# Kernel optimization log

Measured on AMD Instinct MI355X. Metric: run time of the kernel, lower is better.

The kernel has to match this reference:

```python
import jax, jax.numpy as jnp
import numpy as np

V = 100000   # vocab size
H = 1280     # GRU hidden / pic_emb_size
E = 300      # word_emb_size
L = 32       # max_length


def setup_inputs() -> dict:
    key = jax.random.key(0)
    ks = jax.random.split(key, 7)
    s = 0.02  # weight init scale
    return {
        "hidden0": jax.random.normal(ks[0], (H,), jnp.float32),
        "start_emb": jax.random.normal(ks[1], (E,), jnp.float32),
        "W_ih": jax.random.normal(ks[2], (3 * H, E), jnp.float32) * s,
        "W_hh": jax.random.normal(ks[3], (3 * H, H), jnp.float32) * s,
        "b_ih": jnp.zeros((3 * H,), jnp.float32),
        "b_hh": jnp.zeros((3 * H,), jnp.float32),
        "W_cls": jax.random.normal(ks[4], (V, H), jnp.float32) * s,
        "b_cls": jnp.zeros((V,), jnp.float32),
        "vocab_vectors": jax.random.normal(ks[5], (V, E), jnp.float32),
        "max_length": L,
    }


def reference(hidden0, start_emb, W_ih, W_hh, b_ih, b_hh, W_cls, b_cls,
              vocab_vectors, max_length):
    """Autoregressive GRU decode: GRU step -> 1280x100k classifier GEMV ->
    argmax -> embedding gather, for max_length steps (batch=1).
    EOS (token 0) emulated with a `done` mask instead of a Python break.
    Returns (tokens [L] int32, hiddens [L, H] float32)."""

    def step(carry, _):
        h, emb, done = carry
        # PyTorch GRU gate layout: [reset | update | new]
        gi = W_ih @ emb + b_ih               # [3H]
        gh = W_hh @ h + b_hh                 # [3H]
        r = jax.nn.sigmoid(gi[:H] + gh[:H])
        z = jax.nn.sigmoid(gi[H:2 * H] + gh[H:2 * H])
        n = jnp.tanh(gi[2 * H:] + r * gh[2 * H:])
        h_new = jnp.where(done, h, (1.0 - z) * n + z * h)
        logits = W_cls @ h_new + b_cls       # [V] classifier GEMV
        pred = jnp.argmax(logits).astype(jnp.int32)
        token = jnp.where(done, 0, pred)
        done_new = done | (pred == 0)
        emb_new = jnp.where(done_new, emb, vocab_vectors[pred])  # gather next word emb
        return (h_new, emb_new, done_new), (token, h_new)

    init = (hidden0, start_emb, jnp.array(False))
    _, (tokens, hiddens) = jax.lax.scan(step, init, None, length=max_length)
    return tokens, hiddens
```

## Files before the change

### kernel.cpp

```cpp
#include <hip/hip_runtime.h>
#include <math.h>
#include <limits.h>

#define V 100000
#define H 1280
#define E 300
#define L 32
#define NBLK 1563

#define WS_H0     0
#define WS_H1     1280
#define WS_EMB    2560
#define WS_SUM8   2880
#define WS_DONE   3008
#define WS_LOGITS 3012
#define WS_SROW   (WS_LOGITS + V)
#define WS_PLO    (WS_SROW + V)
#define WS_PHI    (WS_PLO + NBLK)
#define WS_Q_BYTEOFF 824576
#define WS_BYTES_NEEDED (WS_Q_BYTEOFF + (size_t)V * H)
#define CAND_CAP  256
#define PBLK_CAP  128

#define FB_GI     4000
#define FB_GH     (FB_GI + 3840)
#define FB_NPART  6250
#define FB_PVAL   12000
#define FB_PIDX   (FB_PVAL + FB_NPART)

__global__ __launch_bounds__(256)
void init_state(const float* __restrict__ hidden0, const float* __restrict__ start_emb,
                float* __restrict__ ws) {
    int i = blockIdx.x * blockDim.x + threadIdx.x;
    if (i < H) ws[WS_H0 + i] = hidden0[i];
    if (i < E) ws[WS_EMB + i] = start_emb[i];
    if (i < 8) ws[WS_SUM8 + i * 16] = 0.f;
    if (i == 0) ((int*)ws)[WS_DONE] = 0;
}

__global__ __launch_bounds__(256)
void convert_int8(const float* __restrict__ W, uint* __restrict__ q_out,
                  float* __restrict__ ws) {
    const int wave = threadIdx.x >> 6;
    const int lane = threadIdx.x & 63;
    const int row = blockIdx.x * 4 + wave;
    const float4* __restrict__ wr = (const float4*)(W + (size_t)row * H);

    float4 v[5];
    float mx = 0.f;
    #pragma unroll
    for (int k = 0; k < 5; ++k) {
        v[k] = wr[lane + 64*k];
        mx = fmaxf(mx, fmaxf(fmaxf(fabsf(v[k].x), fabsf(v[k].y)),
                             fmaxf(fabsf(v[k].z), fabsf(v[k].w))));
    }
    #pragma unroll
    for (int off = 32; off; off >>= 1) mx = fmaxf(mx, __shfl_xor(mx, off));

    float inv = (mx > 0.f) ? 127.0f / mx : 0.f;
    float s   = (mx > 0.f) ? mx / 127.0f : 0.f;

    uint* __restrict__ qrow = q_out + (size_t)row * (H/4);
    #pragma unroll
    for (int k = 0; k < 5; ++k) {
        int q0 = max(-127, min(127, __float2int_rn(v[k].x * inv)));
        int q1 = max(-127, min(127, __float2int_rn(v[k].y * inv)));
        int q2 = max(-127, min(127, __float2int_rn(v[k].z * inv)));
        int q3 = max(-127, min(127, __float2int_rn(v[k].w * inv)));
        qrow[lane + 64*k] = (uint)(q0 & 0xff) | ((uint)(q1 & 0xff) << 8) |
                            ((uint)(q2 & 0xff) << 16) | ((uint)(q3 & 0xff) << 24);
    }
    if (lane == 0) ws[WS_SROW + row] = s;
}

__global__ __launch_bounds__(192)
void gru_fused(const float* __restrict__ W_ih, const float* __restrict__ W_hh,
               const float* __restrict__ b_ih, const float* __restrict__ b_hh,
               float* __restrict__ ws, const float* __restrict__ hin,
               float* __restrict__ hout, float* __restrict__ hid_out) {
    const int g = threadIdx.x >> 6;
    const int lane = threadIdx.x & 63;
    const int j = blockIdx.x;
    const int row = g * H + j;

    const float4* __restrict__ emb4 = (const float4*)(ws + WS_EMB);
    const float4* __restrict__ h4   = (const float4*)hin;

    const float4* __restrict__ wi = (const float4*)(W_ih + (size_t)row * E);
    float si = 0.f;
    for (int i = lane; i < 75; i += 64) {
        float4 w = wi[i], e = emb4[i];
        si += w.x*e.x + w.y*e.y + w.z*e.z + w.w*e.w;
    }
    const float4* __restrict__ wh = (const float4*)(W_hh + (size_t)row * H);
    float sh = 0.f;
    #pragma unroll
    for (int k = 0; k < 5; ++k) {
        float4 w = wh[lane + 64*k], hv = h4[lane + 64*k];
        sh += w.x*hv.x + w.y*hv.y + w.z*hv.z + w.w*hv.w;
    }
    #pragma unroll
    for (int off = 32; off; off >>= 1) {
        si += __shfl_down(si, off);
        sh += __shfl_down(sh, off);
    }
    __shared__ float gi_s[3], gh_s[3];
    if (lane == 0) {
        gi_s[g] = si + b_ih[row];
        gh_s[g] = sh + b_hh[row];
    }
    __syncthreads();
    if (threadIdx.x == 0) {
        float r = 1.f / (1.f + expf(-(gi_s[0] + gh_s[0])));
        float z = 1.f / (1.f + expf(-(gi_s[1] + gh_s[1])));
        float n = tanhf(gi_s[2] + r * gh_s[2]);
        int done = ((const int*)ws)[WS_DONE];
        float hold = hin[j];
        float hnew = done ? hold : (1.f - z) * n + z * hold;
        hout[j] = hnew;
        hid_out[j] = hnew;
        atomicAdd(ws + WS_SUM8 + (j & 7) * 16, fabsf(hnew));
    }
}

__global__ __launch_bounds__(256)
void cls_int8(const uint* __restrict__ Q, const float* __restrict__ b_cls,
              float* __restrict__ ws, const float* __restrict__ h) {
    const int wave = threadIdx.x >> 6;
    const int lane = threadIdx.x & 63;
    const int row0 = blockIdx.x * 64 + wave * 16;
    const float4* __restrict__ h4 = (const float4*)h;

    float4 hv[5];
    #pragma unroll
    for (int k = 0; k < 5; ++k) hv[k] = h4[lane + 64*k];

    float sumabs = 0.f;
    #pragma unroll
    for (int i = 0; i < 8; ++i) sumabs += ws[WS_SUM8 + i * 16];

    float wlo = -INFINITY, whi = -INFINITY;

    for (int rr = 0; rr < 16; ++rr) {
        const int row = row0 + rr;
        if (row >= V) break;
        const uint* __restrict__ qr = Q + (size_t)row * (H/4);
        float acc = 0.f;
        #pragma unroll
        for (int k = 0; k < 5; ++k) {
            uint u = qr[lane + 64*k];
            float f0 = (float)((int)(u << 24) >> 24);
            float f1 = (float)((int)(u << 16) >> 24);
            float f2 = (float)((int)(u <<  8) >> 24);
            float f3 = (float)((int) u        >> 24);
            acc += f0*hv[k].x + f1*hv[k].y + f2*hv[k].z + f3*hv[k].w;
        }
        #pragma unroll
        for (int off = 32; off; off >>= 1) acc += __shfl_down(acc, off);
        if (lane == 0) {
            float s = ws[WS_SROW + row];
            float q = s * acc + b_cls[row];
            ws[WS_LOGITS + row] = q;
            float e = 0.501f * s * sumabs + 0.002f;
            wlo = fmaxf(wlo, q - e);
            whi = fmaxf(whi, q + e);
        }
    }
    __shared__ float slo[4], shi[4];
    if (lane == 0) { slo[wave] = wlo; shi[wave] = whi; }
    __syncthreads();
    if (threadIdx.x == 0) {
        ws[WS_PLO + blockIdx.x] = fmaxf(fmaxf(slo[0], slo[1]), fmaxf(slo[2], slo[3]));
        ws[WS_PHI + blockIdx.x] = fmaxf(fmaxf(shi[0], shi[1]), fmaxf(shi[2], shi[3]));
    }
}

__global__ __launch_bounds__(1024)
void finalize(float* __restrict__ ws, const float* __restrict__ W_cls,
              const float* __restrict__ b_cls, const float* __restrict__ vocab,
              float* __restrict__ tok_out, int t, const float* __restrict__ h) {
    __shared__ float red[1024];
    __shared__ int   npass, cnt;
    __shared__ int   pblk[PBLK_CAP];
    __shared__ int   cidx[CAND_CAP];
    __shared__ float cval[CAND_CAP];
    __shared__ int   s_pred, s_done_new;
    const int tid = threadIdx.x;

    float sumabs = 0.f;
    #pragma unroll
    for (int i = 0; i < 8; ++i) sumabs += ws[WS_SUM8 + i * 16];

    float m = -INFINITY;
    for (int b = tid; b < NBLK; b += 1024) m = fmaxf(m, ws[WS_PLO + b]);
    red[tid] = m;
    __syncthreads();
    for (int s = 512; s; s >>= 1) {
        if (tid < s) red[tid] = fmaxf(red[tid], red[tid + s]);
        __syncthreads();
    }
    m = red[0];
    if (tid == 0) { npass = 0; cnt = 0; }
    __syncthreads();

    for (int b = tid; b < NBLK; b += 1024) {
        if (ws[WS_PHI + b] >= m) {
            int p = atomicAdd(&npass, 1);
            if (p < PBLK_CAP) pblk[p] = b;
        }
    }
    __syncthreads();
    const int np = min(npass, PBLK_CAP);

    for (int k = tid; k < np * 64; k += 1024) {
        int row = pblk[k >> 6] * 64 + (k & 63);
        if (row < V) {
            float s = ws[WS_SROW + row];
            float e = 0.501f * s * sumabs + 0.002f;
            if (ws[WS_LOGITS + row] + e >= m) {
                int p = atomicAdd(&cnt, 1);
                if (p < CAND_CAP) cidx[p] = row;
            }
        }
    }
    __syncthreads();
    const int nc = min(cnt, CAND_CAP);

    const int wave = tid >> 6;
    const int lane = tid & 63;
    const float4* __restrict__ h4 = (const float4*)h;
    for (int c = wave; c < nc; c += 16) {
        int row = cidx[c];
        const float4* __restrict__ wr = (const float4*)(W_cls + (size_t)row * H);
        float s = 0.f;
        #pragma unroll
        for (int k = 0; k < 5; ++k) {
            float4 wv = wr[lane + 64*k], hvv = h4[lane + 64*k];
            s += wv.x*hvv.x + wv.y*hvv.y + wv.z*hvv.z + wv.w*hvv.w;
        }
        #pragma unroll
        for (int off = 32; off; off >>= 1) s += __shfl_down(s, off);
        if (lane == 0) cval[c] = s + b_cls[row];
    }
    __syncthreads();

    if (tid == 0) {
        float bv = -INFINITY; int bi = INT_MAX;
        for (int c = 0; c < nc; ++c) {
            float v = cval[c]; int i = cidx[c];
            if (v > bv || (v == bv && i < bi)) { bv = v; bi = i; }
        }
        int done = ((const int*)ws)[WS_DONE];
        int pred = bi;
        tok_out[t] = (float)(done ? 0 : pred);
        int dn = done | (pred == 0);
        ((int*)ws)[WS_DONE] = dn;
        s_pred = pred; s_done_new = dn;
    }
    __syncthreads();
    if (!s_done_new && tid < E)
        ws[WS_EMB + tid] = vocab[(size_t)s_pred * E + tid];
    if (tid < 8) ws[WS_SUM8 + tid * 16] = 0.f;
}

__global__ __launch_bounds__(256)
void fb_gru_matvec(const float* __restrict__ W_ih, const float* __restrict__ W_hh,
                   const float* __restrict__ b_ih, const float* __restrict__ b_hh,
                   float* __restrict__ ws) {
    const int wave = threadIdx.x >> 6;
    const int lane = threadIdx.x & 63;
    const int row = blockIdx.x * 4 + wave;
    const float4* __restrict__ emb4 = (const float4*)(ws + WS_EMB);
    const float4* __restrict__ h4   = (const float4*)(ws + WS_H0);
    const float4* __restrict__ wi = (const float4*)(W_ih + (size_t)row * E);
    float s1 = 0.f;
    for (int i = lane; i < 75; i += 64) {
        float4 w = wi[i], e = emb4[i];
        s1 += w.x*e.x + w.y*e.y + w.z*e.z + w.w*e.w;
    }
    const float4* __restrict__ wh = (const float4*)(W_hh + (size_t)row * H);
    float s2 = 0.f;
    #pragma unroll
    for (int k = 0; k < 5; ++k) {
        float4 w = wh[lane + 64*k], hv = h4[lane + 64*k];
        s2 += w.x*hv.x + w.y*hv.y + w.z*hv.z + w.w*hv.w;
    }
    #pragma unroll
    for (int off = 32; off; off >>= 1) {
        s1 += __shfl_down(s1, off);
        s2 += __shfl_down(s2, off);
    }
    if (lane == 0) {
        ws[FB_GI + row] = s1 + b_ih[row];
        ws[FB_GH + row] = s2 + b_hh[row];
    }
}

__global__ __launch_bounds__(256)
void fb_gru_combine(float* __restrict__ ws, float* __restrict__ hid_out) {
    int j = blockIdx.x * 256 + threadIdx.x;
    if (j >= H) return;
    int done = ((const int*)ws)[WS_DONE];
    float gir = ws[FB_GI + j], giz = ws[FB_GI + H + j], gin = ws[FB_GI + 2*H + j];
    float ghr = ws[FB_GH + j], ghz = ws[FB_GH + H + j], ghn = ws[FB_GH + 2*H + j];
    float r = 1.f / (1.f + expf(-(gir + ghr)));
    float z = 1.f / (1.f + expf(-(giz + ghz)));
    float n = tanhf(gin + r * ghn);
    float hold = ws[WS_H0 + j];
    float hnew = done ? hold : (1.f - z) * n + z * hold;
    ws[WS_H0 + j] = hnew;
    hid_out[j] = hnew;
}

__global__ __launch_bounds__(256)
void fb_logits_argmax(const float* __restrict__ W_cls, const float* __restrict__ b_cls,
                      float* __restrict__ ws) {
    const int wave = threadIdx.x >> 6;
    const int lane = threadIdx.x & 63;
    const int row0 = blockIdx.x * 16 + wave * 4;
    const float4* __restrict__ h4 = (const float4*)(ws + WS_H0);
    float best = -INFINITY;
    int bidx = INT_MAX;
    for (int rr = 0; rr < 4; ++rr) {
        const int row = row0 + rr;
        const float4* __restrict__ wr = (const float4*)(W_cls + (size_t)row * H);
        float s = 0.f;
        #pragma unroll
        for (int k = 0; k < 5; ++k) {
            float4 w = wr[lane + 64*k], hv = h4[lane + 64*k];
            s += w.x*hv.x + w.y*hv.y + w.z*hv.z + w.w*hv.w;
        }
        #pragma unroll
        for (int off = 32; off; off >>= 1) s += __shfl_down(s, off);
        if (lane == 0) {
            float logit = s + b_cls[row];
            if (logit > best) { best = logit; bidx = row; }
        }
    }
    __shared__ float sval[4];
    __shared__ int   sidx[4];
    if (lane == 0) { sval[wave] = best; sidx[wave] = bidx; }
    __syncthreads();
    if (threadIdx.x == 0) {
        float bv = sval[0]; int bi = sidx[0];
        #pragma unroll
        for (int w = 1; w < 4; ++w)
            if (sval[w] > bv || (sval[w] == bv && sidx[w] < bi)) { bv = sval[w]; bi = sidx[w]; }
        ws[FB_PVAL + blockIdx.x] = bv;
        ((int*)ws)[FB_PIDX + blockIdx.x] = bi;
    }
}

__global__ __launch_bounds__(1024)
void fb_argmax_update(float* __restrict__ ws, const float* __restrict__ vocab,
                      float* __restrict__ tok_out, int t) {
    __shared__ float sval[1024];
    __shared__ int   sidx[1024];
    const int tid = threadIdx.x;
    float best = -INFINITY;
    int bidx = INT_MAX;
    for (int i = tid; i < FB_NPART; i += 1024) {
        float v = ws[FB_PVAL + i];
        int  id = ((const int*)ws)[FB_PIDX + i];
        if (v > best || (v == best && id < bidx)) { best = v; bidx = id; }
    }
    sval[tid] = best; sidx[tid] = bidx;
    __syncthreads();
    #pragma unroll
    for (int s = 512; s; s >>= 1) {
        if (tid < s) {
            if (sval[tid+s] > sval[tid] ||
                (sval[tid+s] == sval[tid] && sidx[tid+s] < sidx[tid])) {
                sval[tid] = sval[tid+s]; sidx[tid] = sidx[tid+s];
            }
        }
        __syncthreads();
    }
    __shared__ int s_pred, s_donenew;
    if (tid == 0) {
        int pred = sidx[0];
        int done = ((const int*)ws)[WS_DONE];
        tok_out[t] = (float)(done ? 0 : pred);
        int done_new = done | (pred == 0);
        ((int*)ws)[WS_DONE] = done_new;
        s_pred = pred; s_donenew = done_new;
    }
    __syncthreads();
    if (!s_donenew && tid < E)
        ws[WS_EMB + tid] = vocab[(size_t)s_pred * E + tid];
}

extern "C" void kernel_launch(void* const* d_in, const int* in_sizes, int n_in,
                              void* d_out, int out_size, void* d_ws, size_t ws_size,
                              hipStream_t stream) {
    const float* hidden0   = (const float*)d_in[0];
    const float* start_emb = (const float*)d_in[1];
    const float* W_ih      = (const float*)d_in[2];
    const float* W_hh      = (const float*)d_in[3];
    const float* b_ih      = (const float*)d_in[4];
    const float* b_hh      = (const float*)d_in[5];
    const float* W_cls     = (const float*)d_in[6];
    const float* b_cls     = (const float*)d_in[7];
    const float* vocab     = (const float*)d_in[8];
    float* out = (float*)d_out;
    float* ws  = (float*)d_ws;

    hipLaunchKernelGGL(init_state, dim3(5), dim3(256), 0, stream, hidden0, start_emb, ws);

    if (ws_size >= WS_BYTES_NEEDED) {
        uint* Q = (uint*)((char*)d_ws + WS_Q_BYTEOFF);
        hipLaunchKernelGGL(convert_int8, dim3(V/4), dim3(256), 0, stream, W_cls, Q, ws);
        for (int t = 0; t < L; ++t) {
            const float* hin = ws + ((t & 1) ? WS_H1 : WS_H0);
            float* hout      = ws + ((t & 1) ? WS_H0 : WS_H1);
            hipLaunchKernelGGL(gru_fused, dim3(H), dim3(192), 0, stream,
                               W_ih, W_hh, b_ih, b_hh, ws, hin, hout,
                               out + L + (size_t)t * H);
            hipLaunchKernelGGL(cls_int8, dim3(NBLK), dim3(256), 0, stream,
                               Q, b_cls, ws, hout);
            hipLaunchKernelGGL(finalize, dim3(1), dim3(1024), 0, stream,
                               ws, W_cls, b_cls, vocab, out, t, hout);
        }
    } else {
        for (int t = 0; t < L; ++t) {
            hipLaunchKernelGGL(fb_gru_matvec, dim3(960), dim3(256), 0, stream,
                               W_ih, W_hh, b_ih, b_hh, ws);
            hipLaunchKernelGGL(fb_gru_combine, dim3(5), dim3(256), 0, stream,
                               ws, out + L + (size_t)t * H);
            hipLaunchKernelGGL(fb_logits_argmax, dim3(FB_NPART), dim3(256), 0, stream,
                               W_cls, b_cls, ws);
            hipLaunchKernelGGL(fb_argmax_update, dim3(1), dim3(1024), 0, stream,
                               ws, vocab, out, t);
        }
    }
}
```

Baseline: 1.539 ms.

## Fuse argmax finalize into next step's GRU kernel, redundantly per block

```diff
diff --git a/kernel.cpp b/kernel.cpp
--- a/kernel.cpp
+++ b/kernel.cpp
@@ -11,16 +11,18 @@
 #define WS_H0     0
 #define WS_H1     1280
 #define WS_EMB    2560
-#define WS_SUM8   2880
-#define WS_DONE   3008
-#define WS_LOGITS 3012
+#define WS_SUMA   2880
+#define WS_SUMB   3008
+#define WS_DONE0  3136
+#define WS_DONE1  3137
+#define WS_LOGITS 3140
 #define WS_SROW   (WS_LOGITS + V)
 #define WS_PLO    (WS_SROW + V)
 #define WS_PHI    (WS_PLO + NBLK)
-#define WS_Q_BYTEOFF 824576
+#define WS_Q_BYTEOFF 825088
 #define WS_BYTES_NEEDED (WS_Q_BYTEOFF + (size_t)V * H)
-#define CAND_CAP  256
-#define PBLK_CAP  128
+#define CAND_CAP 256
+#define PBLK_CAP 128
 
 #define FB_GI     4000
 #define FB_GH     (FB_GI + 3840)
@@ -32,10 +34,10 @@
 void init_state(const float* __restrict__ hidden0, const float* __restrict__ start_emb,
                 float* __restrict__ ws) {
     int i = blockIdx.x * blockDim.x + threadIdx.x;
-    if (i < H) ws[WS_H0 + i] = hidden0[i];
+    if (i < H) { ws[WS_H0 + i] = hidden0[i]; ws[WS_H1 + i] = hidden0[i]; }
     if (i < E) ws[WS_EMB + i] = start_emb[i];
-    if (i < 8) ws[WS_SUM8 + i * 16] = 0.f;
-    if (i == 0) ((int*)ws)[WS_DONE] = 0;
+    if (i < 8) { ws[WS_SUMA + i * 16] = 0.f; ws[WS_SUMB + i * 16] = 0.f; }
+    if (i == 0) { ((int*)ws)[WS_DONE0] = 0; ((int*)ws)[WS_DONE1] = 0; }
 }
 
 __global__ __launch_bounds__(256)
@@ -73,59 +75,165 @@
     if (lane == 0) ws[WS_SROW + row] = s;
 }
 
-__global__ __launch_bounds__(192)
-void gru_fused(const float* __restrict__ W_ih, const float* __restrict__ W_hh,
-               const float* __restrict__ b_ih, const float* __restrict__ b_hh,
-               float* __restrict__ ws, const float* __restrict__ hin,
-               float* __restrict__ hout, float* __restrict__ hid_out) {
-    const int g = threadIdx.x >> 6;
-    const int lane = threadIdx.x & 63;
-    const int j = blockIdx.x;
-    const int row = g * H + j;
-
-    const float4* __restrict__ emb4 = (const float4*)(ws + WS_EMB);
-    const float4* __restrict__ h4   = (const float4*)hin;
-
-    const float4* __restrict__ wi = (const float4*)(W_ih + (size_t)row * E);
-    float si = 0.f;
-    for (int i = lane; i < 75; i += 64) {
-        float4 w = wi[i], e = emb4[i];
-        si += w.x*e.x + w.y*e.y + w.z*e.z + w.w*e.w;
-    }
-    const float4* __restrict__ wh = (const float4*)(W_hh + (size_t)row * H);
-    float sh = 0.f;
-    #pragma unroll
-    for (int k = 0; k < 5; ++k) {
-        float4 w = wh[lane + 64*k], hv = h4[lane + 64*k];
-        sh += w.x*hv.x + w.y*hv.y + w.z*hv.z + w.w*hv.w;
+__global__ __launch_bounds__(256)
+void fin_gru(const float* __restrict__ W_ih, const float* __restrict__ W_hh,
+             const float* __restrict__ b_ih, const float* __restrict__ b_hh,
+             const float* __restrict__ W_cls, const float* __restrict__ b_cls,
+             const float* __restrict__ vocab, const float* __restrict__ start_emb,
+             float* __restrict__ ws, float* __restrict__ out,
+             float* __restrict__ hid_out, int k) {
+    __shared__ float red[256];
+    __shared__ int   npass, cnt;
+    __shared__ int   pblk[PBLK_CAP];
+    __shared__ int   cidx[CAND_CAP];
+    __shared__ float cval[CAND_CAP];
+    __shared__ int   s_pred, s_done;
+    __shared__ __align__(16) float emb_s[304];
+
+    const int tid  = threadIdx.x;
+    const int wave = tid >> 6;
+    const int lane = tid & 63;
+
+    const float* hin  = ws + ((k & 1) ^ 1) * H;
+    float*       hout = ws + (k & 1) * H;
+
+    if (k == 0) {
+        for (int i = tid; i < E; i += 256) emb_s[i] = start_emb[i];
+        if (tid == 0) s_done = 0;
+        __syncthreads();
+    } else {
+        const int sslot = ((k - 1) & 1) ? WS_SUMB : WS_SUMA;
+        float sumabs = 0.f;
+        #pragma unroll
+        for (int i = 0; i < 8; ++i) sumabs += ws[sslot + i * 16];
+
+        float m = -INFINITY;
+        for (int b = tid; b < NBLK; b += 256) m = fmaxf(m, ws[WS_PLO + b]);
+        red[tid] = m;
+        __syncthreads();
+        for (int s = 128; s; s >>= 1) {
+            if (tid < s) red[tid] = fmaxf(red[tid], red[tid + s]);
+            __syncthreads();
+        }
+        m = red[0];
+        if (tid == 0) { npass = 0; cnt = 0; }
+        __syncthreads();
+
+        for (int b = tid; b < NBLK; b += 256) {
+            if (ws[WS_PHI + b] >= m) {
+                int p = atomicAdd(&npass, 1);
+                if (p < PBLK_CAP) pblk[p] = b;
+            }
+        }
+        __syncthreads();
+        const int np = min(npass, PBLK_CAP);
+
+        for (int j = tid; j < np * 64; j += 256) {
+            int row = pblk[j >> 6] * 64 + (j & 63);
+            if (row < V) {
+                float s = ws[WS_SROW + row];
+                float e = 0.501f * s * sumabs + 0.002f;
+                if (ws[WS_LOGITS + row] + e >= m) {
+                    int p = atomicAdd(&cnt, 1);
+                    if (p < CAND_CAP) cidx[p] = row;
+                }
+            }
+        }
+        __syncthreads();
+        const int nc = min(cnt, CAND_CAP);
+
+        const float4* h4r = (const float4*)hin;
+        for (int c = wave; c < nc; c += 4) {
+            int row = cidx[c];
+            const float4* wr = (const float4*)(W_cls + (size_t)row * H);
+            float s = 0.f;
+            #pragma unroll
+            for (int kk = 0; kk < 5; ++kk) {
+                float4 wv = wr[lane + 64*kk], hv = h4r[lane + 64*kk];
+                s += wv.x*hv.x + wv.y*hv.y + wv.z*hv.z + wv.w*hv.w;
+            }
+            #pragma unroll
+            for (int off = 32; off; off >>= 1) s += __shfl_down(s, off);
+            if (lane == 0) cval[c] = s + b_cls[row];
+        }
+        __syncthreads();
+
+        if (tid == 0) {
+            float bv = -INFINITY; int bi = INT_MAX;
+            for (int c = 0; c < nc; ++c) {
+                float v = cval[c]; int i = cidx[c];
+                if (v > bv || (v == bv && i < bi)) { bv = v; bi = i; }
+            }
+            int pred = bi;
+            int done_in = (k >= 2) ? ((const int*)ws)[(k & 1) ? WS_DONE1 : WS_DONE0] : 0;
+            if (blockIdx.x == 0) out[k - 1] = (float)(done_in ? 0 : pred);
+            int dn = done_in | (pred == 0);
+            ((int*)ws)[((k - 1) & 1) ? WS_DONE1 : WS_DONE0] = dn;
+            s_pred = pred; s_done = dn;
+        }
+        __syncthreads();
+        const int pr = s_pred;
+        for (int i = tid; i < E; i += 256) emb_s[i] = vocab[(size_t)pr * E + i];
+        __syncthreads();
+    }
+
+    const int u = blockIdx.x * 4 + wave;
+    const float4* emb4 = (const float4*)emb_s;
+    const float4* h4 = (const float4*)hin;
+    float4 hv[5];
+    #pragma unroll
+    for (int kk = 0; kk < 5; ++kk) hv[kk] = h4[lane + 64*kk];
+
+    float si0 = 0.f, si1 = 0.f, si2 = 0.f, sh0 = 0.f, sh1 = 0.f, sh2 = 0.f;
+    {
+        const float4* w0 = (const float4*)(W_ih + (size_t)u * E);
+        const float4* w1 = (const float4*)(W_ih + (size_t)(H + u) * E);
+        const float4* w2 = (const float4*)(W_ih + (size_t)(2*H + u) * E);
+        for (int i = lane; i < 75; i += 64) {
+            float4 e = emb4[i];
+            float4 a = w0[i]; si0 += a.x*e.x + a.y*e.y + a.z*e.z + a.w*e.w;
+            float4 b = w1[i]; si1 += b.x*e.x + b.y*e.y + b.z*e.z + b.w*e.w;
+            float4 c = w2[i]; si2 += c.x*e.x + c.y*e.y + c.z*e.z + c.w*e.w;
+        }
+        const float4* v0 = (const float4*)(W_hh + (size_t)u * H);
+        const float4* v1 = (const float4*)(W_hh + (size_t)(H + u) * H);
+        const float4* v2 = (const float4*)(W_hh + (size_t)(2*H + u) * H);
+        #pragma unroll
+        for (int kk = 0; kk < 5; ++kk) {
+            float4 a = v0[lane + 64*kk];
+            sh0 += a.x*hv[kk].x + a.y*hv[kk].y + a.z*hv[kk].z + a.w*hv[kk].w;
+            float4 b = v1[lane + 64*kk];
+            sh1 += b.x*hv[kk].x + b.y*hv[kk].y + b.z*hv[kk].z + b.w*hv[kk].w;
+            float4 c = v2[lane + 64*kk];
+            sh2 += c.x*hv[kk].x + c.y*hv[kk].y + c.z*hv[kk].z + c.w*hv[kk].w;
+        }
     }
     #pragma unroll
     for (int off = 32; off; off >>= 1) {
-        si += __shfl_down(si, off);
-        sh += __shfl_down(sh, off);
-    }
-    __shared__ float gi_s[3], gh_s[3];
+        si0 += __shfl_down(si0, off); si1 += __shfl_down(si1, off);
+        si2 += __shfl_down(si2, off);
+        sh0 += __shfl_down(sh0, off); sh1 += __shfl_down(sh1, off);
+        sh2 += __shfl_down(sh2, off);
+    }
     if (lane == 0) {
-        gi_s[g] = si + b_ih[row];
-        gh_s[g] = sh + b_hh[row];
-    }
-    __syncthreads();
-    if (threadIdx.x == 0) {
-        float r = 1.f / (1.f + expf(-(gi_s[0] + gh_s[0])));
-        float z = 1.f / (1.f + expf(-(gi_s[1] + gh_s[1])));
-        float n = tanhf(gi_s[2] + r * gh_s[2]);
-        int done = ((const int*)ws)[WS_DONE];
-        float hold = hin[j];
-        float hnew = done ? hold : (1.f - z) * n + z * hold;
-        hout[j] = hnew;
-        hid_out[j] = hnew;
-        atomicAdd(ws + WS_SUM8 + (j & 7) * 16, fabsf(hnew));
+        float r = 1.f / (1.f + expf(-(si0 + b_ih[u]       + sh0 + b_hh[u])));
+        float z = 1.f / (1.f + expf(-(si1 + b_ih[H + u]   + sh1 + b_hh[H + u])));
+        float n = tanhf(si2 + b_ih[2*H + u] + r * (sh2 + b_hh[2*H + u]));
+        float hold = hin[u];
+        float hnew = s_done ? hold : (1.f - z) * n + z * hold;
+        hout[u] = hnew;
+        hid_out[u] = hnew;
+        const int aslot = (k & 1) ? WS_SUMB : WS_SUMA;
+        atomicAdd(ws + aslot + (u & 7) * 16, fabsf(hnew));
     }
 }
 
 __global__ __launch_bounds__(256)
 void cls_int8(const uint* __restrict__ Q, const float* __restrict__ b_cls,
-              float* __restrict__ ws, const float* __restrict__ h) {
+              float* __restrict__ ws, const float* __restrict__ h, int k) {
+    if (blockIdx.x == 0 && threadIdx.x < 8)
+        ws[(((k + 1) & 1) ? WS_SUMB : WS_SUMA) + threadIdx.x * 16] = 0.f;
+
     const int wave = threadIdx.x >> 6;
     const int lane = threadIdx.x & 63;
     const int row0 = blockIdx.x * 64 + wave * 16;
@@ -133,27 +241,27 @@
 
     float4 hv[5];
     #pragma unroll
-    for (int k = 0; k < 5; ++k) hv[k] = h4[lane + 64*k];
-
+    for (int kk = 0; kk < 5; ++kk) hv[kk] = h4[lane + 64*kk];
+
+    const int sslot = (k & 1) ? WS_SUMB : WS_SUMA;
     float sumabs = 0.f;
     #pragma unroll
-    for (int i = 0; i < 8; ++i) sumabs += ws[WS_SUM8 + i * 16];
+    for (int i = 0; i < 8; ++i) sumabs += ws[sslot + i * 16];
 
     float wlo = -INFINITY, whi = -INFINITY;
-
     for (int rr = 0; rr < 16; ++rr) {
         const int row = row0 + rr;
         if (row >= V) break;
         const uint* __restrict__ qr = Q + (size_t)row * (H/4);
         float acc = 0.f;
         #pragma unroll
-        for (int k = 0; k < 5; ++k) {
-            uint u = qr[lane + 64*k];
+        for (int kk = 0; kk < 5; ++kk) {
+            uint u = qr[lane + 64*kk];
             float f0 = (float)((int)(u << 24) >> 24);
             float f1 = (float)((int)(u << 16) >> 24);
             float f2 = (float)((int)(u <<  8) >> 24);
             float f3 = (float)((int) u        >> 24);
-            acc += f0*hv[k].x + f1*hv[k].y + f2*hv[k].z + f3*hv[k].w;
+            acc += f0*hv[kk].x + f1*hv[kk].y + f2*hv[kk].z + f3*hv[kk].w;
         }
         #pragma unroll
         for (int off = 32; off; off >>= 1) acc += __shfl_down(acc, off);
@@ -175,27 +283,26 @@
     }
 }
 
-__global__ __launch_bounds__(1024)
-void finalize(float* __restrict__ ws, const float* __restrict__ W_cls,
-              const float* __restrict__ b_cls, const float* __restrict__ vocab,
-              float* __restrict__ tok_out, int t, const float* __restrict__ h) {
-    __shared__ float red[1024];
+__global__ __launch_bounds__(256)
+void finalize_tail(float* __restrict__ ws, const float* __restrict__ W_cls,
+                   const float* __restrict__ b_cls, float* __restrict__ out) {
+    __shared__ float red[256];
     __shared__ int   npass, cnt;
     __shared__ int   pblk[PBLK_CAP];
     __shared__ int   cidx[CAND_CAP];
     __shared__ float cval[CAND_CAP];
-    __shared__ int   s_pred, s_done_new;
     const int tid = threadIdx.x;
+    const int wave = tid >> 6, lane = tid & 63;
 
     float sumabs = 0.f;
     #pragma unroll
-    for (int i = 0; i < 8; ++i) sumabs += ws[WS_SUM8 + i * 16];
+    for (int i = 0; i < 8; ++i) sumabs += ws[WS_SUMB + i * 16];
 
     float m = -INFINITY;
-    for (int b = tid; b < NBLK; b += 1024) m = fmaxf(m, ws[WS_PLO + b]);
+    for (int b = tid; b < NBLK; b += 256) m = fmaxf(m, ws[WS_PLO + b]);
     red[tid] = m;
     __syncthreads();
-    for (int s = 512; s; s >>= 1) {
+    for (int s = 128; s; s >>= 1) {
         if (tid < s) red[tid] = fmaxf(red[tid], red[tid + s]);
         __syncthreads();
     }
@@ -203,7 +310,7 @@
     if (tid == 0) { npass = 0; cnt = 0; }
     __syncthreads();
 
-    for (int b = tid; b < NBLK; b += 1024) {
+    for (int b = tid; b < NBLK; b += 256) {
         if (ws[WS_PHI + b] >= m) {
             int p = atomicAdd(&npass, 1);
             if (p < PBLK_CAP) pblk[p] = b;
@@ -212,8 +319,8 @@
     __syncthreads();
     const int np = min(npass, PBLK_CAP);
 
-    for (int k = tid; k < np * 64; k += 1024) {
-        int row = pblk[k >> 6] * 64 + (k & 63);
+    for (int j = tid; j < np * 64; j += 256) {
+        int row = pblk[j >> 6] * 64 + (j & 63);
         if (row < V) {
             float s = ws[WS_SROW + row];
             float e = 0.501f * s * sumabs + 0.002f;
@@ -226,17 +333,15 @@
     __syncthreads();
     const int nc = min(cnt, CAND_CAP);
 
-    const int wave = tid >> 6;
-    const int lane = tid & 63;
-    const float4* __restrict__ h4 = (const float4*)h;
-    for (int c = wave; c < nc; c += 16) {
+    const float4* h4 = (const float4*)(ws + WS_H1);
+    for (int c = wave; c < nc; c += 4) {
         int row = cidx[c];
-        const float4* __restrict__ wr = (const float4*)(W_cls + (size_t)row * H);
+        const float4* wr = (const float4*)(W_cls + (size_t)row * H);
         float s = 0.f;
         #pragma unroll
-        for (int k = 0; k < 5; ++k) {
-            float4 wv = wr[lane + 64*k], hvv = h4[lane + 64*k];
-            s += wv.x*hvv.x + wv.y*hvv.y + wv.z*hvv.z + wv.w*hvv.w;
+        for (int kk = 0; kk < 5; ++kk) {
+            float4 wv = wr[lane + 64*kk], hv = h4[lane + 64*kk];
+            s += wv.x*hv.x + wv.y*hv.y + wv.z*hv.z + wv.w*hv.w;
         }
         #pragma unroll
         for (int off = 32; off; off >>= 1) s += __shfl_down(s, off);
@@ -250,17 +355,9 @@
             float v = cval[c]; int i = cidx[c];
             if (v > bv || (v == bv && i < bi)) { bv = v; bi = i; }
         }
-        int done = ((const int*)ws)[WS_DONE];
-        int pred = bi;
-        tok_out[t] = (float)(done ? 0 : pred);
-        int dn = done | (pred == 0);
-        ((int*)ws)[WS_DONE] = dn;
-        s_pred = pred; s_done_new = dn;
-    }
-    __syncthreads();
-    if (!s_done_new && tid < E)
-        ws[WS_EMB + tid] = vocab[(size_t)s_pred * E + tid];
-    if (tid < 8) ws[WS_SUM8 + tid * 16] = 0.f;
+        int done_in = ((const int*)ws)[WS_DONE0];
+        out[L - 1] = (float)(done_in ? 0 : bi);
+    }
 }
 
 __global__ __launch_bounds__(256)
@@ -300,7 +397,7 @@
 void fb_gru_combine(float* __restrict__ ws, float* __restrict__ hid_out) {
     int j = blockIdx.x * 256 + threadIdx.x;
     if (j >= H) return;
-    int done = ((const int*)ws)[WS_DONE];
+    int done = ((const int*)ws)[WS_DONE0];
     float gir = ws[FB_GI + j], giz = ws[FB_GI + H + j], gin = ws[FB_GI + 2*H + j];
     float ghr = ws[FB_GH + j], ghz = ws[FB_GH + H + j], ghn = ws[FB_GH + 2*H + j];
     float r = 1.f / (1.f + expf(-(gir + ghr)));
@@ -379,10 +476,10 @@
     __shared__ int s_pred, s_donenew;
     if (tid == 0) {
         int pred = sidx[0];
-        int done = ((const int*)ws)[WS_DONE];
+        int done = ((const int*)ws)[WS_DONE0];
         tok_out[t] = (float)(done ? 0 : pred);
         int done_new = done | (pred == 0);
-        ((int*)ws)[WS_DONE] = done_new;
+        ((int*)ws)[WS_DONE0] = done_new;
         s_pred = pred; s_donenew = done_new;
     }
     __syncthreads();
@@ -410,17 +507,16 @@
     if (ws_size >= WS_BYTES_NEEDED) {
         uint* Q = (uint*)((char*)d_ws + WS_Q_BYTEOFF);
         hipLaunchKernelGGL(convert_int8, dim3(V/4), dim3(256), 0, stream, W_cls, Q, ws);
-        for (int t = 0; t < L; ++t) {
-            const float* hin = ws + ((t & 1) ? WS_H1 : WS_H0);
-            float* hout      = ws + ((t & 1) ? WS_H0 : WS_H1);
-            hipLaunchKernelGGL(gru_fused, dim3(H), dim3(192), 0, stream,
-                               W_ih, W_hh, b_ih, b_hh, ws, hin, hout,
-                               out + L + (size_t)t * H);
+        for (int k = 0; k < L; ++k) {
+            const float* hk = ws + (k & 1) * H;
+            hipLaunchKernelGGL(fin_gru, dim3(H/4), dim3(256), 0, stream,
+                               W_ih, W_hh, b_ih, b_hh, W_cls, b_cls, vocab,
+                               start_emb, ws, out, out + L + (size_t)k * H, k);
             hipLaunchKernelGGL(cls_int8, dim3(NBLK), dim3(256), 0, stream,
-                               Q, b_cls, ws, hout);
-            hipLaunchKernelGGL(finalize, dim3(1), dim3(1024), 0, stream,
-                               ws, W_cls, b_cls, vocab, out, t, hout);
-        }
+                               Q, b_cls, ws, hk, k);
+        }
+        hipLaunchKernelGGL(finalize_tail, dim3(1), dim3(256), 0, stream,
+                           ws, W_cls, b_cls, out);
     } else {
         for (int t = 0; t < L; ++t) {
             hipLaunchKernelGGL(fb_gru_matvec, dim3(960), dim3(256), 0, stream,
```

Measured after the change: 1.670 ms. +8.5%, slower.

## Compute W_hh·h gate projections inside classifier kernel instead of GRU step

Applied to the files above, without the earlier changes.

```diff
diff --git a/kernel.cpp b/kernel.cpp
--- a/kernel.cpp
+++ b/kernel.cpp
@@ -7,20 +7,22 @@
 #define E 300
 #define L 32
 #define NBLK 1563
+#define GHBLK 320
 
 #define WS_H0     0
 #define WS_H1     1280
 #define WS_EMB    2560
 #define WS_SUM8   2880
 #define WS_DONE   3008
-#define WS_LOGITS 3012
+#define WS_GH     3072
+#define WS_LOGITS 6912
 #define WS_SROW   (WS_LOGITS + V)
 #define WS_PLO    (WS_SROW + V)
 #define WS_PHI    (WS_PLO + NBLK)
-#define WS_Q_BYTEOFF 824576
+#define WS_Q_BYTEOFF 840192
 #define WS_BYTES_NEEDED (WS_Q_BYTEOFF + (size_t)V * H)
-#define CAND_CAP  256
-#define PBLK_CAP  128
+#define CAND_CAP 256
+#define PBLK_CAP 128
 
 #define FB_GI     4000
 #define FB_GH     (FB_GI + 3840)
@@ -40,9 +42,34 @@
 
 __global__ __launch_bounds__(256)
 void convert_int8(const float* __restrict__ W, uint* __restrict__ q_out,
-                  float* __restrict__ ws) {
+                  float* __restrict__ ws, const float* __restrict__ W_hh,
+                  const float* __restrict__ b_hh) {
     const int wave = threadIdx.x >> 6;
     const int lane = threadIdx.x & 63;
+
+    if (blockIdx.x >= V/4) {
+        const int tb = (blockIdx.x - V/4) * 4 + wave;
+        const float4* h4 = (const float4*)(ws + WS_H0);
+        float4 hv[5];
+        #pragma unroll
+        for (int k = 0; k < 5; ++k) hv[k] = h4[lane + 64*k];
+        #pragma unroll
+        for (int rr = 0; rr < 3; ++rr) {
+            const int row = tb * 3 + rr;
+            const float4* wr = (const float4*)(W_hh + (size_t)row * H);
+            float s = 0.f;
+            #pragma unroll
+            for (int k = 0; k < 5; ++k) {
+                float4 w = wr[lane + 64*k];
+                s += w.x*hv[k].x + w.y*hv[k].y + w.z*hv[k].z + w.w*hv[k].w;
+            }
+            #pragma unroll
+            for (int off = 32; off; off >>= 1) s += __shfl_down(s, off);
+            if (lane == 0) ws[WS_GH + row] = s + b_hh[row];
+        }
+        return;
+    }
+
     const int row = blockIdx.x * 4 + wave;
     const float4* __restrict__ wr = (const float4*)(W + (size_t)row * H);
 
@@ -74,8 +101,7 @@
 }
 
 __global__ __launch_bounds__(192)
-void gru_fused(const float* __restrict__ W_ih, const float* __restrict__ W_hh,
-               const float* __restrict__ b_ih, const float* __restrict__ b_hh,
+void gru_fused(const float* __restrict__ W_ih, const float* __restrict__ b_ih,
                float* __restrict__ ws, const float* __restrict__ hin,
                float* __restrict__ hout, float* __restrict__ hid_out) {
     const int g = threadIdx.x >> 6;
@@ -84,36 +110,22 @@
     const int row = g * H + j;
 
     const float4* __restrict__ emb4 = (const float4*)(ws + WS_EMB);
-    const float4* __restrict__ h4   = (const float4*)hin;
-
     const float4* __restrict__ wi = (const float4*)(W_ih + (size_t)row * E);
     float si = 0.f;
     for (int i = lane; i < 75; i += 64) {
         float4 w = wi[i], e = emb4[i];
         si += w.x*e.x + w.y*e.y + w.z*e.z + w.w*e.w;
     }
-    const float4* __restrict__ wh = (const float4*)(W_hh + (size_t)row * H);
-    float sh = 0.f;
-    #pragma unroll
-    for (int k = 0; k < 5; ++k) {
-        float4 w = wh[lane + 64*k], hv = h4[lane + 64*k];
-        sh += w.x*hv.x + w.y*hv.y + w.z*hv.z + w.w*hv.w;
-    }
-    #pragma unroll
-    for (int off = 32; off; off >>= 1) {
-        si += __shfl_down(si, off);
-        sh += __shfl_down(sh, off);
-    }
-    __shared__ float gi_s[3], gh_s[3];
-    if (lane == 0) {
-        gi_s[g] = si + b_ih[row];
-        gh_s[g] = sh + b_hh[row];
-    }
+    #pragma unroll
+    for (int off = 32; off; off >>= 1) si += __shfl_down(si, off);
+
+    __shared__ float gi_s[3];
+    if (lane == 0) gi_s[g] = si + b_ih[row];
     __syncthreads();
     if (threadIdx.x == 0) {
-        float r = 1.f / (1.f + expf(-(gi_s[0] + gh_s[0])));
-        float z = 1.f / (1.f + expf(-(gi_s[1] + gh_s[1])));
-        float n = tanhf(gi_s[2] + r * gh_s[2]);
+        float r = 1.f / (1.f + expf(-(gi_s[0] + ws[WS_GH + j])));
+        float z = 1.f / (1.f + expf(-(gi_s[1] + ws[WS_GH + H + j])));
+        float n = tanhf(gi_s[2] + r * ws[WS_GH + 2*H + j]);
         int done = ((const int*)ws)[WS_DONE];
         float hold = hin[j];
         float hnew = done ? hold : (1.f - z) * n + z * hold;
@@ -125,35 +137,61 @@
 
 __global__ __launch_bounds__(256)
 void cls_int8(const uint* __restrict__ Q, const float* __restrict__ b_cls,
-              float* __restrict__ ws, const float* __restrict__ h) {
+              float* __restrict__ ws, const float* __restrict__ h,
+              const float* __restrict__ W_hh, const float* __restrict__ b_hh,
+              int last) {
     const int wave = threadIdx.x >> 6;
     const int lane = threadIdx.x & 63;
+
+    if (blockIdx.x >= NBLK) {
+        if (last) return;
+        const int tb = (blockIdx.x - NBLK) * 4 + wave;
+        const float4* h4 = (const float4*)h;
+        float4 hv[5];
+        #pragma unroll
+        for (int k = 0; k < 5; ++k) hv[k] = h4[lane + 64*k];
+        #pragma unroll
+        for (int rr = 0; rr < 3; ++rr) {
+            const int row = tb * 3 + rr;
+            const float4* wr = (const float4*)(W_hh + (size_t)row * H);
+            float s = 0.f;
+            #pragma unroll
+            for (int k = 0; k < 5; ++k) {
+                float4 w = wr[lane + 64*k];
+                s += w.x*hv[k].x + w.y*hv[k].y + w.z*hv[k].z + w.w*hv[k].w;
+            }
+            #pragma unroll
+            for (int off = 32; off; off >>= 1) s += __shfl_down(s, off);
+            if (lane == 0) ws[WS_GH + row] = s + b_hh[row];
+        }
+        return;
+    }
+
     const int row0 = blockIdx.x * 64 + wave * 16;
     const float4* __restrict__ h4 = (const float4*)h;
 
     float4 hv[5];
     #pragma unroll
-    for (int k = 0; k < 5; ++k) hv[k] = h4[lane + 64*k];
+    for (int kk = 0; kk < 5; ++kk) hv[kk] = h4[lane + 64*kk];
 
     float sumabs = 0.f;
     #pragma unroll
     for (int i = 0; i < 8; ++i) sumabs += ws[WS_SUM8 + i * 16];
 
     float wlo = -INFINITY, whi = -INFINITY;
-
     for (int rr = 0; rr < 16; ++rr) {
         const int row = row0 + rr;
         if (row >= V) break;
         const uint* __restrict__ qr = Q + (size_t)row * (H/4);
         float acc = 0.f;
         #pragma unroll
-        for (int k = 0; k < 5; ++k) {
-            uint u = qr[lane + 64*k];
+        for (int kk = 0; kk < 5; ++kk) {
+            uint u = qr[lane + 64*kk];
             float f0 = (float)((int)(u << 24) >> 24);
             float f1 = (float)((int)(u << 16) >> 24);
             float f2 = (float)((int)(u <<  8) >> 24);
             float f3 = (float)((int) u        >> 24);
-            acc += f0*hv[k].x + f1*hv[k].y + f2*hv[k].z + f3*hv[k].w;
+            acc += f0*hv[kk].x + f1*hv[kk].y + f2*hv[kk].z + f3*hv[kk].w;
         }
         #pragma unroll
         for (int off = 32; off; off >>= 1) acc += __shfl_down(acc, off);
@@ -409,17 +447,17 @@
 
     if (ws_size >= WS_BYTES_NEEDED) {
         uint* Q = (uint*)((char*)d_ws + WS_Q_BYTEOFF);
-        hipLaunchKernelGGL(convert_int8, dim3(V/4), dim3(256), 0, stream, W_cls, Q, ws);
-        for (int t = 0; t < L; ++t) {
-            const float* hin = ws + ((t & 1) ? WS_H1 : WS_H0);
-            float* hout      = ws + ((t & 1) ? WS_H0 : WS_H1);
+        hipLaunchKernelGGL(convert_int8, dim3(V/4 + GHBLK), dim3(256), 0, stream,
+                           W_cls, Q, ws, W_hh, b_hh);
+        for (int k = 0; k < L; ++k) {
+            const float* hin = ws + ((k & 1) ? WS_H1 : WS_H0);
+            float* hout      = ws + ((k & 1) ? WS_H0 : WS_H1);
             hipLaunchKernelGGL(gru_fused, dim3(H), dim3(192), 0, stream,
-                               W_ih, W_hh, b_ih, b_hh, ws, hin, hout,
-                               out + L + (size_t)t * H);
-            hipLaunchKernelGGL(cls_int8, dim3(NBLK), dim3(256), 0, stream,
-                               Q, b_cls, ws, hout);
+                               W_ih, b_ih, ws, hin, hout, out + L + (size_t)k * H);
+            hipLaunchKernelGGL(cls_int8, dim3(NBLK + GHBLK), dim3(256), 0, stream,
+                               Q, b_cls, ws, hout, W_hh, b_hh, (k == L - 1) ? 1 : 0);
             hipLaunchKernelGGL(finalize, dim3(1), dim3(1024), 0, stream,
-                               ws, W_cls, b_cls, vocab, out, t, hout);
+                               ws, W_cls, b_cls, vocab, out, k, hout);
         }
     } else {
         for (int t = 0; t < L; ++t) {
```

New measurement: 1.573 ms. 2.2% more time.
